# Performance work log

Hardware: AMD Instinct MI355X
Metric: run time of the kernel (lower is better)

## Reference

```python
import jax, jax.numpy as jnp
import numpy as np

# Static problem sizes
N, NS, E, B = 6000, 20000, 60000, 16   # atoms, subgraph nodes, subgraph edges, molecules
IN_DIM, EMB, HID = 78, 1024, 2048
H = 4                 # GAT heads
C = HID // H          # 512 per-head channels
L = 3                 # num GAT layers
LN_EPS = 1e-5
SM_EPS = 1e-16        # PyG softmax denominator eps


def setup_inputs() -> dict:
    key = jax.random.key(0)
    ks = jax.random.split(key, 20)
    g = lambda k, shape, s: jax.random.normal(k, shape, jnp.float32) * s
    inp = {}
    inp["x"] = jax.random.uniform(ks[0], (N, IN_DIM), jnp.float32)
    inp["subgraph_edge_attr"] = jnp.ones((E, 1), jnp.float32)
    inp["Wn"] = g(ks[1], (IN_DIM, EMB), 0.1)
    inp["bn"] = g(ks[2], (EMB,), 0.02)
    inp["We"] = g(ks[3], (1, EMB), 0.1)
    inp["be"] = g(ks[4], (EMB,), 0.02)
    inp["W0"] = g(ks[5], (EMB, HID), EMB ** -0.5)
    inp["Ws"] = g(ks[6], (L - 1, HID, HID), HID ** -0.5)
    inp["att_src"] = g(ks[7], (L, H, C), C ** -0.5)
    inp["att_dst"] = g(ks[8], (L, H, C), C ** -0.5)
    inp["att_edge"] = g(ks[9], (L, H, C), C ** -0.5)
    inp["W_edge"] = g(ks[10], (L, EMB, HID), EMB ** -0.5)
    inp["conv_bias"] = g(ks[11], (L, HID), 0.02)
    inp["gamma"] = jnp.ones((L, HID), jnp.float32)
    inp["beta"] = jnp.zeros((L, HID), jnp.float32)
    inp["Wf"] = g(ks[12], (HID, HID), HID ** -0.5)
    inp["bf"] = g(ks[13], (HID,), 0.02)
    inp["subgraph_node_index"] = jax.random.randint(ks[14], (NS,), 0, N)
    inp["subgraph_edge_index"] = jax.random.randint(ks[15], (2, E), 0, NS)
    inp["subgraph_indicator"] = jax.random.randint(ks[16], (NS,), 0, N)
    inp["batch_index"] = jnp.sort(jax.random.randint(ks[17], (N,), 0, B))
    return inp


def _layernorm(h, g, b):
    mu = h.mean(-1, keepdims=True)
    v = jnp.square(h - mu).mean(-1, keepdims=True)
    return (h - mu) * jax.lax.rsqrt(v + LN_EPS) * g + b


def _gat_conv(h, Win, e_emb, a_src, a_dst, a_edge, We_l, bias, src, dst, n_nodes):
    # h: [n, in]; e_emb: [Et, EMB]; a_*: [H, C]
    xh = (h @ Win).reshape(-1, H, C)                       # [n, H, C]
    s_src = (xh * a_src).sum(-1)                           # [n, H]
    s_dst = (xh * a_dst).sum(-1)                           # [n, H]
    eh = (e_emb @ We_l).reshape(-1, H, C)                  # [Et, H, C]
    s_edge = (eh * a_edge).sum(-1)                         # [Et, H]
    logits = jax.nn.leaky_relu(s_src[src] + s_dst[dst] + s_edge, 0.2)
    # softmax over incoming edges of each destination node, per head
    m = jax.ops.segment_max(logits, dst, num_segments=n_nodes)
    p = jnp.exp(logits - m[dst])
    z = jax.ops.segment_sum(p, dst, num_segments=n_nodes)
    alpha = p / (z[dst] + SM_EPS)                          # [Et, H]
    msg = xh[src] * alpha[:, :, None]                      # [Et, H, C]
    out = jax.ops.segment_sum(msg, dst, num_segments=n_nodes)
    return out.reshape(-1, H * C) + bias                   # [n, HID]


def reference(x, subgraph_edge_attr, Wn, bn, We, be, W0, Ws, att_src, att_dst,
              att_edge, W_edge, conv_bias, gamma, beta, Wf, bf,
              subgraph_node_index, subgraph_edge_index, subgraph_indicator,
              batch_index):
    n_sub = subgraph_node_index.shape[0]
    n_nodes = x.shape[0]
    # node_projection + gather into subgraph-node space
    h = (x @ Wn + bn)[subgraph_node_index]                 # [NS, EMB]
    # edge_encoder
    e = subgraph_edge_attr @ We + be                       # [E, EMB]
    src = subgraph_edge_index[0]
    dst = subgraph_edge_index[1]
    # PyG GATConv add_self_loops with fill_value='mean' on encoded edge attrs
    loop = jnp.arange(n_sub)
    src = jnp.concatenate([src, loop])
    dst = jnp.concatenate([dst, loop])
    e_loop = jnp.broadcast_to(e.mean(axis=0, keepdims=True), (n_sub, e.shape[1]))
    e = jnp.concatenate([e, e_loop], axis=0)               # [E+NS, EMB]
    for i in range(L):
        Win = W0 if i == 0 else Ws[i - 1]
        h = _gat_conv(h, Win, e, att_src[i], att_dst[i], att_edge[i],
                      W_edge[i], conv_bias[i], src, dst, n_sub)
        h = jax.nn.relu(_layernorm(h, gamma[i], beta[i]))
    # subgraph mean aggregation back to atoms (index_add + bincount clamp(1))
    agg = jax.ops.segment_sum(h, subgraph_indicator, num_segments=n_nodes)
    cnt = jax.ops.segment_sum(jnp.ones((n_sub,), h.dtype), subgraph_indicator,
                              num_segments=n_nodes)
    agg = agg / jnp.maximum(cnt, 1.0)[:, None]
    out_nodes = agg @ Wf + bf                              # final_projection
    # global_mean_pool over molecules
    pooled = jax.ops.segment_sum(out_nodes, batch_index, num_segments=B)
    gcnt = jax.ops.segment_sum(jnp.ones((n_nodes,), h.dtype), batch_index,
                               num_segments=B)
    return pooled / jnp.maximum(gcnt, 1.0)[:, None]        # [B, HID]
```

## Files before the change

kernel.cpp:

```cpp
#include <hip/hip_runtime.h>

typedef unsigned short ushortT;
typedef __attribute__((ext_vector_type(4))) float f32x4;
typedef __attribute__((ext_vector_type(8))) short bf16x8;
typedef __attribute__((ext_vector_type(4))) unsigned int u32x4;
typedef __attribute__((ext_vector_type(4))) unsigned short u16x4;

#define N_ATOMS 6000
#define NSUB    20000
#define NEDGE   60000
#define NBATCH  16
#define INDIM   78
#define EMB     1024
#define HID     2048
#define NH      4
#define CH      512
#define NL      3
#define MP      20096
#define AP      6016
#define ETOT    (NEDGE + NSUB)
#define NPB     8

#define GLOAD_LDS16(gp, lp) \
    __builtin_amdgcn_global_load_lds((const __attribute__((address_space(1))) void*)(gp), \
                                     (__attribute__((address_space(3))) void*)(lp), 16, 0, 0)

__device__ __forceinline__ ushortT f2bf(float x) {
    union { float f; unsigned u; } v; v.f = x;
    unsigned r = v.u + 0x7fffu + ((v.u >> 16) & 1u);
    return (ushortT)(r >> 16);
}
__device__ __forceinline__ float bf2f(ushortT h) {
    union { unsigned u; float f; } v; v.u = ((unsigned)h) << 16; return v.f;
}

__global__ void k_cast_transpose(const float* __restrict__ W, ushortT* __restrict__ Wt,
                                 int K, int Nn) {
    __shared__ float tile[32][33];
    int n0 = blockIdx.x * 32, k0 = blockIdx.y * 32;
    int tx = threadIdx.x, ty = threadIdx.y;
    for (int i = 0; i < 32; i += 8)
        tile[ty + i][tx] = W[(size_t)(k0 + ty + i) * Nn + n0 + tx];
    __syncthreads();
    for (int i = 0; i < 32; i += 8)
        Wt[(size_t)(n0 + ty + i) * K + k0 + tx] = f2bf(tile[tx][ty + i]);
}

__global__ __launch_bounds__(256) void k_node_proj(const float* __restrict__ x,
                                                   const float* __restrict__ Wn,
                                                   const float* __restrict__ bn,
                                                   ushortT* __restrict__ xpb) {
    int n0 = blockIdx.x * NPB;
    __shared__ float xr[NPB][INDIM];
    int tid = threadIdx.x;
    for (int i = tid; i < NPB * INDIM; i += 256)
        xr[i / INDIM][i % INDIM] = x[(size_t)(n0 + i / INDIM) * INDIM + (i % INDIM)];
    __syncthreads();
    for (int j = tid; j < EMB; j += 256) {
        float acc[NPB];
        float b = bn[j];
        #pragma unroll
        for (int a = 0; a < NPB; ++a) acc[a] = b;
        #pragma unroll 6
        for (int k = 0; k < INDIM; ++k) {
            float wv = Wn[(size_t)k * EMB + j];
            #pragma unroll
            for (int a = 0; a < NPB; ++a) acc[a] += xr[a][k] * wv;
        }
        #pragma unroll
        for (int a = 0; a < NPB; ++a)
            xpb[(size_t)(n0 + a) * EMB + j] = f2bf(acc[a]);
    }
}

__global__ void k_mean_part(const float* __restrict__ ea, float* __restrict__ mpart) {
    __shared__ float red[256];
    int b = blockIdx.x;
    float s = 0;
    for (int i = b * 256 + threadIdx.x; i < NEDGE; i += 64 * 256) s += ea[i];
    red[threadIdx.x] = s; __syncthreads();
    for (int d = 128; d > 0; d >>= 1) {
        if (threadIdx.x < d) red[threadIdx.x] += red[threadIdx.x + d];
        __syncthreads();
    }
    if (threadIdx.x == 0) mpart[b] = red[0];
}

__global__ void k_eprep(const int* __restrict__ srci, const int* __restrict__ sni,
                        const float* __restrict__ ea, const float* __restrict__ meana,
                        int* __restrict__ esrcS, int* __restrict__ esrcA,
                        float* __restrict__ eaf) {
    int t = blockIdx.x * 256 + threadIdx.x;
    if (t >= ETOT) return;
    int s = (t < NEDGE) ? srci[t] : (t - NEDGE);
    esrcS[t] = s;
    esrcA[t] = sni[s];
    eaf[t] = (t < NEDGE) ? ea[t] : meana[0];
}

__global__ __launch_bounds__(256) void k_pq_part(const float* __restrict__ We,
                                                 const float* __restrict__ be,
                                                 const float* __restrict__ W_edge,
                                                 const float* __restrict__ att_edge,
                                                 float* __restrict__ part) {
    int l = blockIdx.x >> 2, h = blockIdx.x & 3;
    int k0 = blockIdx.y * 64;
    const float* Wl = W_edge + (size_t)l * EMB * HID + h * CH;
    const float* ae = att_edge + ((size_t)l * NH + h) * CH;
    int tid = threadIdx.x;
    float aP0 = 0, aP1 = 0, aQ0 = 0, aQ1 = 0;
    #pragma unroll 4
    for (int k = k0; k < k0 + 64; ++k) {
        float wek = We[k], bek = be[k];
        float w0 = Wl[(size_t)k * HID + tid];
        float w1 = Wl[(size_t)k * HID + tid + 256];
        aP0 += wek * w0; aP1 += wek * w1;
        aQ0 += bek * w0; aQ1 += bek * w1;
    }
    float p = aP0 * ae[tid] + aP1 * ae[tid + 256];
    float q = aQ0 * ae[tid] + aQ1 * ae[tid + 256];
    __shared__ float rp[256], rq[256];
    rp[tid] = p; rq[tid] = q; __syncthreads();
    for (int d = 128; d > 0; d >>= 1) {
        if (tid < d) { rp[tid] += rp[tid + d]; rq[tid] += rq[tid + d]; }
        __syncthreads();
    }
    if (tid == 0) {
        part[((size_t)blockIdx.y * 12 + blockIdx.x) * 2]     = rp[0];
        part[((size_t)blockIdx.y * 12 + blockIdx.x) * 2 + 1] = rq[0];
    }
}

__global__ void k_pq_red(const float* __restrict__ part, const float* __restrict__ mpart,
                         float* __restrict__ pq, float* __restrict__ meana) {
    int t = threadIdx.x;
    if (t < 24) {
        float s = 0;
        for (int kc = 0; kc < 16; ++kc) s += part[((size_t)kc * 12 + (t >> 1)) * 2 + (t & 1)];
        pq[t] = s;
    }
    if (t == 32) {
        float s = 0;
        for (int i = 0; i < 64; ++i) s += mpart[i];
        meana[0] = s / (float)NEDGE;
    }
}

__global__ void k_count(const int* __restrict__ dsti, int* __restrict__ cnt) {
    int t = blockIdx.x * 256 + threadIdx.x;
    if (t >= ETOT) return;
    int d = (t < NEDGE) ? dsti[t] : (t - NEDGE);
    atomicAdd(&cnt[d], 1);
}

__global__ void k_scan(const int* __restrict__ cnt, int* __restrict__ rs, int n) {
    __shared__ int part[1024];
    int tid = threadIdx.x;
    const int per = (n + 1023) / 1024;
    int base = tid * per;
    int s = 0;
    for (int i = 0; i < per; ++i) { int idx = base + i; if (idx < n) s += cnt[idx]; }
    part[tid] = s;
    __syncthreads();
    for (int d = 1; d < 1024; d <<= 1) {
        int v = (tid >= d) ? part[tid - d] : 0;
        __syncthreads();
        part[tid] += v;
        __syncthreads();
    }
    int off = part[tid] - s;
    for (int i = 0; i < per; ++i) {
        int idx = base + i;
        if (idx < n) { rs[idx] = off; off += cnt[idx]; }
    }
    if (tid == 1023) rs[n] = part[1023];
}

__global__ void k_fill(const int* __restrict__ dsti, const int* __restrict__ rs,
                       int* __restrict__ cursor, int* __restrict__ eids) {
    int t = blockIdx.x * 256 + threadIdx.x;
    if (t >= ETOT) return;
    int d = (t < NEDGE) ? dsti[t] : (t - NEDGE);
    int pos = rs[d] + atomicAdd(&cursor[d], 1);
    eids[pos] = t;
}

__global__ void k_count_ind(const int* __restrict__ ind, int* __restrict__ cnt) {
    int i = blockIdx.x * 256 + threadIdx.x;
    if (i < NSUB) atomicAdd(&cnt[ind[i]], 1);
}

__global__ void k_fill_ind(const int* __restrict__ ind, const int* __restrict__ rs,
                           int* __restrict__ cursor, int* __restrict__ ids) {
    int i = blockIdx.x * 256 + threadIdx.x;
    if (i >= NSUB) return;
    int a = ind[i];
    int pos = rs[a] + atomicAdd(&cursor[a], 1);
    ids[pos] = i;
}

__global__ __launch_bounds__(256) void k_gemm(const ushortT* __restrict__ A,
                                              const ushortT* __restrict__ Bt,
                                              ushortT* __restrict__ Cb, int K) {
    __shared__ alignas(16) ushortT As[128 * 64];
    __shared__ alignas(16) ushortT Bs[128 * 64];
    const int tid = threadIdx.x;
    const int nx = (int)gridDim.x;
    const int ny = (int)gridDim.y;
    int o = (int)blockIdx.y * nx + (int)blockIdx.x;
    int cpx = (nx * ny) >> 3;
    int s = (o & 7) * cpx + (o >> 3);
    const int bm = s / ny, bn = s % ny;
    const int wave = tid >> 6, lane = tid & 63;
    const int wr = wave >> 1, wc = wave & 1;
    f32x4 acc[4][4] = {};
    const int frow = lane & 15;
    const int cb0  = lane >> 4;
    const ushortT* Ab = A + (size_t)bm * 128 * K;
    const ushortT* Bb = Bt + (size_t)bn * 128 * K;
    const int srow = (lane >> 3);
    const int sswz = (((lane & 7) ^ srow) << 3);
    for (int k0 = 0; k0 < K; k0 += 64) {
        #pragma unroll
        for (int i = 0; i < 4; ++i) {
            int c = wave * 4 + i;
            int r = c * 8 + srow;
            GLOAD_LDS16(Ab + (size_t)r * K + k0 + sswz, As + c * 512 + lane * 8);
            GLOAD_LDS16(Bb + (size_t)r * K + k0 + sswz, Bs + c * 512 + lane * 8);
        }
        __syncthreads();
        #pragma unroll
        for (int kk = 0; kk < 64; kk += 32) {
            bf16x8 af[4], bfr[4];
            #pragma unroll
            for (int m = 0; m < 4; ++m) {
                int row = wr * 64 + m * 16 + frow;
                int cb = (kk >> 3) + cb0;
                af[m] = *(const bf16x8*)&As[row * 64 + ((cb ^ (frow & 7)) << 3)];
            }
            #pragma unroll
            for (int n = 0; n < 4; ++n) {
                int row = wc * 64 + n * 16 + frow;
                int cb = (kk >> 3) + cb0;
                bfr[n] = *(const bf16x8*)&Bs[row * 64 + ((cb ^ (frow & 7)) << 3)];
            }
            #pragma unroll
            for (int m = 0; m < 4; ++m)
                #pragma unroll
                for (int n = 0; n < 4; ++n)
                    acc[m][n] = __builtin_amdgcn_mfma_f32_16x16x32_bf16(af[m], bfr[n], acc[m][n], 0, 0, 0);
        }
        __syncthreads();
    }
    const int cr = (lane >> 4) * 4;
    const int cc = lane & 15;
    #pragma unroll
    for (int m = 0; m < 4; ++m)
        #pragma unroll
        for (int n = 0; n < 4; ++n)
            #pragma unroll
            for (int r = 0; r < 4; ++r) {
                size_t row = (size_t)bm * 128 + wr * 64 + m * 16 + cr + r;
                int col = bn * 128 + wc * 64 + n * 16 + cc;
                Cb[row * HID + col] = f2bf(acc[m][n][r]);
            }
}

__global__ __launch_bounds__(256) void k_sdots(const ushortT* __restrict__ xh,
                                               const float* __restrict__ att_src,
                                               const float* __restrict__ att_dst,
                                               float* __restrict__ ssrc,
                                               float* __restrict__ sdst, int layer) {
    int n = blockIdx.x;
    int h = threadIdx.x >> 6, lane = threadIdx.x & 63;
    const ushortT* row = xh + (size_t)n * HID + h * CH + lane * 8;
    const float* as = att_src + ((size_t)layer * NH + h) * CH + lane * 8;
    const float* ad = att_dst + ((size_t)layer * NH + h) * CH + lane * 8;
    u16x4 v0 = *(const u16x4*)row, v1 = *(const u16x4*)(row + 4);
    f32x4 a0 = *(const f32x4*)as, a1 = *(const f32x4*)(as + 4);
    f32x4 d0 = *(const f32x4*)ad, d1 = *(const f32x4*)(ad + 4);
    float ps = 0.f, pd = 0.f;
    #pragma unroll
    for (int t = 0; t < 4; ++t) {
        float f0 = bf2f(v0[t]), f1 = bf2f(v1[t]);
        ps += f0 * a0[t] + f1 * a1[t];
        pd += f0 * d0[t] + f1 * d1[t];
    }
    #pragma unroll
    for (int d = 32; d > 0; d >>= 1) { ps += __shfl_down(ps, d); pd += __shfl_down(pd, d); }
    if (lane == 0) { ssrc[n * NH + h] = ps; sdst[n * NH + h] = pd; }
}

__global__ __launch_bounds__(256) void k_attn(const ushortT* __restrict__ xh,
                                              const float* __restrict__ ssrc,
                                              const float* __restrict__ sdst,
                                              const int* __restrict__ rs,
                                              const int* __restrict__ eids,
                                              const int* __restrict__ esrc,
                                              const float* __restrict__ eaf,
                                              const float* __restrict__ pq,
                                              const float* __restrict__ conv_bias,
                                              const float* __restrict__ gammav,
                                              const float* __restrict__ betav,
                                              ushortT* __restrict__ hout, int layer,
                                              const int* __restrict__ nmap) {
    int n = blockIdx.x;
    int h = threadIdx.x >> 6, lane = threadIdx.x & 63;
    int nn = nmap ? nmap[n] : n;
    int beg = rs[n], end = rs[n + 1];
    float px = pq[(layer * NH + h) * 2], qx = pq[(layer * NH + h) * 2 + 1];
    float sd = sdst[nn * NH + h];
    float m = -INFINITY, z = 0.f;
    float facc[8] = {0, 0, 0, 0, 0, 0, 0, 0};
    for (int pos = beg; pos < end; ++pos) {
        int t = eids[pos];
        int s = esrc[t];
        float logit = ssrc[s * NH + h] + sd + eaf[t] * px + qx;
        logit = (logit > 0.f) ? logit : 0.2f * logit;
        float mn = fmaxf(m, logit);
        float scale = expf(m - mn);
        float w = expf(logit - mn);
        z = z * scale + w;
        const ushortT* xr = xh + (size_t)s * HID + h * CH + lane * 8;
        u16x4 u0 = *(const u16x4*)xr, u1 = *(const u16x4*)(xr + 4);
        #pragma unroll
        for (int j = 0; j < 4; ++j) {
            facc[j]     = facc[j]     * scale + w * bf2f(u0[j]);
            facc[4 + j] = facc[4 + j] * scale + w * bf2f(u1[j]);
        }
        m = mn;
    }
    float inv = 1.f / (z + 1e-16f);
    int cbase = h * CH + lane * 8;
    float val[8], s1 = 0.f, s2 = 0.f;
    #pragma unroll
    for (int j = 0; j < 8; ++j) {
        float v = facc[j] * inv + conv_bias[layer * HID + cbase + j];
        val[j] = v; s1 += v; s2 += v * v;
    }
    __shared__ float r1[256], r2[256];
    r1[threadIdx.x] = s1; r2[threadIdx.x] = s2; __syncthreads();
    for (int d = 128; d > 0; d >>= 1) {
        if (threadIdx.x < d) { r1[threadIdx.x] += r1[threadIdx.x + d]; r2[threadIdx.x] += r2[threadIdx.x + d]; }
        __syncthreads();
    }
    float mu = r1[0] / (float)HID;
    float var = r2[0] / (float)HID - mu * mu;
    float rstd = rsqrtf(var + 1e-5f);
    #pragma unroll
    for (int j = 0; j < 8; ++j) {
        int c = cbase + j;
        float y = (val[j] - mu) * rstd * gammav[layer * HID + c] + betav[layer * HID + c];
        y = fmaxf(y, 0.f);
        hout[(size_t)n * HID + c] = f2bf(y);
    }
}

__global__ __launch_bounds__(256) void k_agg(const ushortT* __restrict__ hbf,
                                             const int* __restrict__ rs2,
                                             const int* __restrict__ ids2,
                                             float* __restrict__ agg) {
    int a = blockIdx.x;
    int beg = rs2[a], end = rs2[a + 1];
    int col = threadIdx.x * 8;
    float acc[8] = {0,0,0,0,0,0,0,0};
    for (int pos = beg; pos < end; ++pos) {
        int i = ids2[pos];
        const u16x4* ptr = (const u16x4*)(hbf + (size_t)i * HID + col);
        u16x4 h0 = ptr[0], h1 = ptr[1];
        #pragma unroll
        for (int t = 0; t < 4; ++t) { acc[t] += bf2f(h0[t]); acc[4 + t] += bf2f(h1[t]); }
    }
    int cnt = end - beg;
    float inv = 1.f / (float)(cnt > 1 ? cnt : 1);
    f32x4 o0, o1;
    #pragma unroll
    for (int t = 0; t < 4; ++t) { o0[t] = acc[t] * inv; o1[t] = acc[4 + t] * inv; }
    float* dst = agg + (size_t)a * HID + col;
    *(f32x4*)dst = o0;
    *(f32x4*)(dst + 4) = o1;
}

__global__ void k_branges(const int* __restrict__ batch, int* __restrict__ bstart,
                          int* __restrict__ bend) {
    int a = blockIdx.x * 256 + threadIdx.x;
    if (a < N_ATOMS) {
        int b = batch[a];
        atomicMin(&bstart[b], a);
        atomicMax(&bend[b], a + 1);
    }
}

__global__ __launch_bounds__(128) void k_pool(const float* __restrict__ agg,
                                              const int* __restrict__ bstart,
                                              const int* __restrict__ bend,
                                              float* __restrict__ pa) {
    int b = blockIdx.x;
    int col = blockIdx.y * 128 + threadIdx.x;
    int s = bstart[b], e = bend[b];
    float v = 0.f;
    for (int a = s; a < e; ++a) v += agg[(size_t)a * HID + col];
    int g = e - s;
    pa[b * HID + col] = (g > 0) ? v / (float)g : 0.f;
}

__global__ __launch_bounds__(256) void k_fpart(const float* __restrict__ pa,
                                               const float* __restrict__ Wf,
                                               float* __restrict__ part) {
    int kc = blockIdx.x;
    int col = blockIdx.y * 256 + threadIdx.x;
    int k0 = kc * 128;
    __shared__ float pl[NBATCH][128];
    for (int i = threadIdx.x; i < NBATCH * 128; i += 256) {
        int b = i >> 7, k = i & 127;
        pl[b][k] = pa[b * HID + k0 + k];
    }
    __syncthreads();
    float acc[NBATCH];
    #pragma unroll
    for (int b = 0; b < NBATCH; ++b) acc[b] = 0.f;
    for (int kk = 0; kk < 128; kk += 4) {
        f32x4 w;
        #pragma unroll
        for (int u = 0; u < 4; ++u) w[u] = Wf[(size_t)(k0 + kk + u) * HID + col];
        #pragma unroll
        for (int b = 0; b < NBATCH; ++b) {
            f32x4 pv = *(const f32x4*)&pl[b][kk];
            acc[b] += pv[0] * w[0] + pv[1] * w[1] + pv[2] * w[2] + pv[3] * w[3];
        }
    }
    #pragma unroll
    for (int b = 0; b < NBATCH; ++b)
        part[((size_t)kc * NBATCH + b) * HID + col] = acc[b];
}

__global__ __launch_bounds__(256) void k_fred(const float* __restrict__ part,
                                              const float* __restrict__ bfv,
                                              const int* __restrict__ bstart,
                                              const int* __restrict__ bend,
                                              float* __restrict__ out) {
    int b = blockIdx.x;
    int col = blockIdx.y * 256 + threadIdx.x;
    float s = 0.f;
    #pragma unroll
    for (int kc = 0; kc < 16; ++kc)
        s += part[((size_t)kc * NBATCH + b) * HID + col];
    int g = bend[b] - bstart[b];
    out[b * HID + col] = (g > 0) ? s + bfv[col] : 0.f;
}

extern "C" void kernel_launch(void* const* d_in, const int* in_sizes, int n_in,
                              void* d_out, int out_size, void* d_ws, size_t ws_size,
                              hipStream_t stream) {
    const float* x         = (const float*)d_in[0];
    const float* ea        = (const float*)d_in[1];
    const float* Wn        = (const float*)d_in[2];
    const float* bn        = (const float*)d_in[3];
    const float* We        = (const float*)d_in[4];
    const float* be        = (const float*)d_in[5];
    const float* W0        = (const float*)d_in[6];
    const float* Ws        = (const float*)d_in[7];
    const float* att_src   = (const float*)d_in[8];
    const float* att_dst   = (const float*)d_in[9];
    const float* att_edge  = (const float*)d_in[10];
    const float* W_edge    = (const float*)d_in[11];
    const float* conv_bias = (const float*)d_in[12];
    const float* gammav    = (const float*)d_in[13];
    const float* betav     = (const float*)d_in[14];
    const float* Wf        = (const float*)d_in[15];
    const float* bfv       = (const float*)d_in[16];
    const int* sni         = (const int*)d_in[17];
    const int* sei         = (const int*)d_in[18];
    const int* sind        = (const int*)d_in[19];
    const int* batch       = (const int*)d_in[20];
    float* out = (float*)d_out;

    char* p = (char*)d_ws;
    auto carve = [&](size_t bytes) -> char* {
        char* r = p; p += (bytes + 255) & ~(size_t)255; return r;
    };
    ushortT* Wt0   = (ushortT*)carve((size_t)HID * EMB * 2);
    ushortT* Wt1   = (ushortT*)carve((size_t)HID * HID * 2);
    ushortT* Wt2   = (ushortT*)carve((size_t)HID * HID * 2);
    ushortT* xpb   = (ushortT*)carve((size_t)AP * EMB * 2);
    ushortT* xha   = (ushortT*)carve((size_t)AP * HID * 2);
    ushortT* hbf   = (ushortT*)carve((size_t)MP * HID * 2);
    ushortT* xhb   = (ushortT*)carve((size_t)MP * HID * 2);
    float*   ssrc  = (float*)carve((size_t)MP * NH * 4);
    float*   sdstb = (float*)carve((size_t)MP * NH * 4);
    float*   ssrca = (float*)carve((size_t)AP * NH * 4);
    float*   sdsta = (float*)carve((size_t)AP * NH * 4);
    float*   pq    = (float*)carve(NL * NH * 2 * 4);
    float*   meana = (float*)carve(256);
    float*   pqpart= (float*)carve((size_t)16 * 12 * 2 * 4);
    float*   mpart = (float*)carve(64 * 4);
    int*     cntdeg= (int*)carve((size_t)NSUB * 4);
    int*     rs    = (int*)carve((size_t)(NSUB + 1) * 4);
    int*     cursor= (int*)carve((size_t)NSUB * 4);
    int*     eids  = (int*)carve((size_t)ETOT * 4);
    int*     esrcS = (int*)carve((size_t)ETOT * 4);
    int*     esrcA = (int*)carve((size_t)ETOT * 4);
    float*   eaf   = (float*)carve((size_t)ETOT * 4);
    int*     cnt2  = (int*)carve((size_t)N_ATOMS * 4);
    int*     rs2   = (int*)carve((size_t)(N_ATOMS + 1) * 4);
    int*     cur2  = (int*)carve((size_t)N_ATOMS * 4);
    int*     ids2  = (int*)carve((size_t)NSUB * 4);
    int*     bstart= (int*)carve(NBATCH * 4);
    int*     bend  = (int*)carve(NBATCH * 4);
    float*   pa    = (float*)carve((size_t)NBATCH * HID * 4);
    float*   part  = (float*)carve((size_t)16 * NBATCH * HID * 4);
    float*   agg   = (float*)xhb;

    hipMemsetAsync(hbf + (size_t)NSUB * HID, 0, (size_t)(MP - NSUB) * HID * 2, stream);
    hipMemsetAsync(xpb + (size_t)N_ATOMS * EMB, 0, (size_t)(AP - N_ATOMS) * EMB * 2, stream);
    hipMemsetAsync(cntdeg, 0, (size_t)NSUB * 4, stream);
    hipMemsetAsync(cursor, 0, (size_t)NSUB * 4, stream);
    hipMemsetAsync(cnt2, 0, (size_t)N_ATOMS * 4, stream);
    hipMemsetAsync(cur2, 0, (size_t)N_ATOMS * 4, stream);
    hipMemsetAsync(bstart, 0x7f, NBATCH * 4, stream);
    hipMemsetAsync(bend, 0, NBATCH * 4, stream);

    dim3 tb(32, 8);
    k_cast_transpose<<<dim3(HID / 32, EMB / 32), tb, 0, stream>>>(W0, Wt0, EMB, HID);
    k_cast_transpose<<<dim3(HID / 32, HID / 32), tb, 0, stream>>>(Ws, Wt1, HID, HID);
    k_cast_transpose<<<dim3(HID / 32, HID / 32), tb, 0, stream>>>(Ws + (size_t)HID * HID, Wt2, HID, HID);

    k_node_proj<<<N_ATOMS / NPB, 256, 0, stream>>>(x, Wn, bn, xpb);
    k_mean_part<<<64, 256, 0, stream>>>(ea, mpart);
    k_pq_part<<<dim3(NL * NH, 16), 256, 0, stream>>>(We, be, W_edge, att_edge, pqpart);
    k_pq_red<<<1, 64, 0, stream>>>(pqpart, mpart, pq, meana);

    const int* dsti = sei + NEDGE;
    k_eprep<<<(ETOT + 255) / 256, 256, 0, stream>>>(sei, sni, ea, meana, esrcS, esrcA, eaf);
    k_count<<<(ETOT + 255) / 256, 256, 0, stream>>>(dsti, cntdeg);
    k_scan<<<1, 1024, 0, stream>>>(cntdeg, rs, NSUB);
    k_fill<<<(ETOT + 255) / 256, 256, 0, stream>>>(dsti, rs, cursor, eids);
    k_count_ind<<<(NSUB + 255) / 256, 256, 0, stream>>>(sind, cnt2);
    k_scan<<<1, 1024, 0, stream>>>(cnt2, rs2, N_ATOMS);
    k_fill_ind<<<(NSUB + 255) / 256, 256, 0, stream>>>(sind, rs2, cur2, ids2);
    k_branges<<<(N_ATOMS + 255) / 256, 256, 0, stream>>>(batch, bstart, bend);

    k_gemm<<<dim3(AP / 128, HID / 128), 256, 0, stream>>>(xpb, Wt0, xha, EMB);
    k_sdots<<<N_ATOMS, 256, 0, stream>>>(xha, att_src, att_dst, ssrca, sdsta, 0);
    k_attn<<<NSUB, 256, 0, stream>>>(xha, ssrca, sdsta, rs, eids, esrcA, eaf, pq,
                                     conv_bias, gammav, betav, hbf, 0, sni);

    for (int l = 1; l < NL; ++l) {
        const ushortT* Wt = (l == 1) ? Wt1 : Wt2;
        k_gemm<<<dim3(MP / 128, HID / 128), 256, 0, stream>>>(hbf, Wt, xhb, HID);
        k_sdots<<<NSUB, 256, 0, stream>>>(xhb, att_src, att_dst, ssrc, sdstb, l);
        k_attn<<<NSUB, 256, 0, stream>>>(xhb, ssrc, sdstb, rs, eids, esrcS, eaf, pq,
                                         conv_bias, gammav, betav, hbf, l, (const int*)nullptr);
    }

    k_agg<<<N_ATOMS, 256, 0, stream>>>(hbf, rs2, ids2, agg);
    k_pool<<<dim3(NBATCH, HID / 128), 128, 0, stream>>>(agg, bstart, bend, pa);
    k_fpart<<<dim3(16, HID / 256), 256, 0, stream>>>(pa, Wf, part);
    k_fred<<<dim3(NBATCH, HID / 256), 256, 0, stream>>>(part, bfv, bstart, bend, out);
}
```

Measured before the change: 987.2 us.

## Map one wavefront per node in GAT attention, replacing block-wide LayerNorm reduction

The attention kernel now gives each 64-lane wavefront a whole destination node, covering all four heads, so one 256-thread block handles four nodes. The shared-memory tree reduction with many __syncthreads for LayerNorm becomes a wavefront shuffle reduction. Edge metadata loads are shared across heads, and bias, gamma, beta and output accesses are vectorized. The trade-off is more registers per thread (4x8 accumulators plus values) and serial per-edge work across heads within a wave. That could lower occupancy, and uneven degrees across the four nodes in a block could leave waves idle.

```diff
diff --git a/kernel.cpp b/kernel.cpp
--- a/kernel.cpp
+++ b/kernel.cpp
@@ -304,55 +304,77 @@
                                               const float* __restrict__ betav,
                                               ushortT* __restrict__ hout, int layer,
                                               const int* __restrict__ nmap) {
-    int n = blockIdx.x;
-    int h = threadIdx.x >> 6, lane = threadIdx.x & 63;
+    int wv = threadIdx.x >> 6, lane = threadIdx.x & 63;
+    int n = blockIdx.x * 4 + wv;
     int nn = nmap ? nmap[n] : n;
     int beg = rs[n], end = rs[n + 1];
-    float px = pq[(layer * NH + h) * 2], qx = pq[(layer * NH + h) * 2 + 1];
-    float sd = sdst[nn * NH + h];
-    float m = -INFINITY, z = 0.f;
-    float facc[8] = {0, 0, 0, 0, 0, 0, 0, 0};
+    float px[NH], qx[NH], sd[NH], m[NH], z[NH];
+    #pragma unroll
+    for (int h = 0; h < NH; ++h) {
+        px[h] = pq[(layer * NH + h) * 2];
+        qx[h] = pq[(layer * NH + h) * 2 + 1];
+        sd[h] = sdst[nn * NH + h];
+        m[h] = -INFINITY; z[h] = 0.f;
+    }
+    float facc[NH][8] = {};
     for (int pos = beg; pos < end; ++pos) {
         int t = eids[pos];
         int s = esrc[t];
-        float logit = ssrc[s * NH + h] + sd + eaf[t] * px + qx;
-        logit = (logit > 0.f) ? logit : 0.2f * logit;
-        float mn = fmaxf(m, logit);
-        float scale = expf(m - mn);
-        float w = expf(logit - mn);
-        z = z * scale + w;
-        const ushortT* xr = xh + (size_t)s * HID + h * CH + lane * 8;
-        u16x4 u0 = *(const u16x4*)xr, u1 = *(const u16x4*)(xr + 4);
+        float a = eaf[t];
+        const ushortT* xr = xh + (size_t)s * HID + lane * 8;
+        #pragma unroll
+        for (int h = 0; h < NH; ++h) {
+            float logit = ssrc[s * NH + h] + sd[h] + a * px[h] + qx[h];
+            logit = (logit > 0.f) ? logit : 0.2f * logit;
+            float mn = fmaxf(m[h], logit);
+            float scale = expf(m[h] - mn);
+            float w = expf(logit - mn);
+            z[h] = z[h] * scale + w;
+            bf16x8 u = *(const bf16x8*)(xr + h * CH);
+            #pragma unroll
+            for (int j = 0; j < 8; ++j)
+                facc[h][j] = facc[h][j] * scale + w * bf2f((ushortT)u[j]);
+            m[h] = mn;
+        }
+    }
+    float val[NH][8];
+    float s1 = 0.f, s2 = 0.f;
+    #pragma unroll
+    for (int h = 0; h < NH; ++h) {
+        float inv = 1.f / (z[h] + 1e-16f);
+        int cb = h * CH + lane * 8;
+        f32x4 b0 = *(const f32x4*)&conv_bias[layer * HID + cb];
+        f32x4 b1 = *(const f32x4*)&conv_bias[layer * HID + cb + 4];
         #pragma unroll
         for (int j = 0; j < 4; ++j) {
-            facc[j]     = facc[j]     * scale + w * bf2f(u0[j]);
-            facc[4 + j] = facc[4 + j] * scale + w * bf2f(u1[j]);
-        }
-        m = mn;
-    }
-    float inv = 1.f / (z + 1e-16f);
-    int cbase = h * CH + lane * 8;
-    float val[8], s1 = 0.f, s2 = 0.f;
-    #pragma unroll
-    for (int j = 0; j < 8; ++j) {
-        float v = facc[j] * inv + conv_bias[layer * HID + cbase + j];
-        val[j] = v; s1 += v; s2 += v * v;
-    }
-    __shared__ float r1[256], r2[256];
-    r1[threadIdx.x] = s1; r2[threadIdx.x] = s2; __syncthreads();
-    for (int d = 128; d > 0; d >>= 1) {
-        if (threadIdx.x < d) { r1[threadIdx.x] += r1[threadIdx.x + d]; r2[threadIdx.x] += r2[threadIdx.x + d]; }
-        __syncthreads();
-    }
-    float mu = r1[0] / (float)HID;
-    float var = r2[0] / (float)HID - mu * mu;
+            float v0 = facc[h][j] * inv + b0[j];
+            float v1 = facc[h][4 + j] * inv + b1[j];
+            val[h][j] = v0; val[h][4 + j] = v1;
+            s1 += v0 + v1; s2 += v0 * v0 + v1 * v1;
+        }
+    }
+    #pragma unroll
+    for (int d = 32; d > 0; d >>= 1) { s1 += __shfl_xor(s1, d); s2 += __shfl_xor(s2, d); }
+    float mu = s1 / (float)HID;
+    float var = s2 / (float)HID - mu * mu;
     float rstd = rsqrtf(var + 1e-5f);
     #pragma unroll
-    for (int j = 0; j < 8; ++j) {
-        int c = cbase + j;
-        float y = (val[j] - mu) * rstd * gammav[layer * HID + c] + betav[layer * HID + c];
-        y = fmaxf(y, 0.f);
-        hout[(size_t)n * HID + c] = f2bf(y);
+    for (int h = 0; h < NH; ++h) {
+        int cb = h * CH + lane * 8;
+        f32x4 g0 = *(const f32x4*)&gammav[layer * HID + cb];
+        f32x4 g1 = *(const f32x4*)&gammav[layer * HID + cb + 4];
+        f32x4 e0 = *(const f32x4*)&betav[layer * HID + cb];
+        f32x4 e1 = *(const f32x4*)&betav[layer * HID + cb + 4];
+        u16x4 o0, o1;
+        #pragma unroll
+        for (int j = 0; j < 4; ++j) {
+            float y0 = (val[h][j] - mu) * rstd * g0[j] + e0[j];
+            float y1 = (val[h][4 + j] - mu) * rstd * g1[j] + e1[j];
+            o0[j] = f2bf(fmaxf(y0, 0.f));
+            o1[j] = f2bf(fmaxf(y1, 0.f));
+        }
+        *(u16x4*)&hout[(size_t)n * HID + cb]     = o0;
+        *(u16x4*)&hout[(size_t)n * HID + cb + 4] = o1;
     }
 }
 
@@ -542,15 +564,15 @@
 
     k_gemm<<<dim3(AP / 128, HID / 128), 256, 0, stream>>>(xpb, Wt0, xha, EMB);
     k_sdots<<<N_ATOMS, 256, 0, stream>>>(xha, att_src, att_dst, ssrca, sdsta, 0);
-    k_attn<<<NSUB, 256, 0, stream>>>(xha, ssrca, sdsta, rs, eids, esrcA, eaf, pq,
-                                     conv_bias, gammav, betav, hbf, 0, sni);
+    k_attn<<<NSUB / 4, 256, 0, stream>>>(xha, ssrca, sdsta, rs, eids, esrcA, eaf, pq,
+                                         conv_bias, gammav, betav, hbf, 0, sni);
 
     for (int l = 1; l < NL; ++l) {
         const ushortT* Wt = (l == 1) ? Wt1 : Wt2;
         k_gemm<<<dim3(MP / 128, HID / 128), 256, 0, stream>>>(hbf, Wt, xhb, HID);
         k_sdots<<<NSUB, 256, 0, stream>>>(xhb, att_src, att_dst, ssrc, sdstb, l);
-        k_attn<<<NSUB, 256, 0, stream>>>(xhb, ssrc, sdstb, rs, eids, esrcS, eaf, pq,
-                                         conv_bias, gammav, betav, hbf, l, (const int*)nullptr);
+        k_attn<<<NSUB / 4, 256, 0, stream>>>(xhb, ssrc, sdstb, rs, eids, esrcS, eaf, pq,
+                                             conv_bias, gammav, betav, hbf, l, (const int*)nullptr);
     }
 
     k_agg<<<N_ATOMS, 256, 0, stream>>>(hbf, rs2, ids2, agg);
```

Result: no change. 997.2 us (+1.0%).
